# Optimization experiments

Measured on AMD Instinct MI355X. Metric: run time of the kernel, lower is better.

Reference implementation:

```python
import jax, jax.numpy as jnp
import numpy as np
import math

N, C_IN, H, W = 8, 256, 64, 64
C_ATT, C_OUT = 128, 256
BN_EPS = 1e-5


def conv_bn_relu(x, w, gamma, beta, mean, var):
    # 1x1 conv (no bias) + BatchNorm (eval mode) + ReLU
    y = jnp.einsum('oc,nchw->nohw', w, x)
    inv = gamma / jnp.sqrt(var + BN_EPS)
    y = y * inv[None, :, None, None] + (beta - mean * inv)[None, :, None, None]
    return jax.nn.relu(y)


def setup_inputs() -> dict:
    key = jax.random.key(0)
    ks = jax.random.split(key, 12)
    x = jax.random.normal(ks[0], (N, C_IN, H, W), dtype=jnp.float32)
    mask = jnp.ones((N, 1, H, W), dtype=jnp.float32)
    reduc_w = jax.random.normal(ks[1], (C_OUT, C_IN), dtype=jnp.float32) * (1.0 / math.sqrt(C_IN))
    reduc_gamma = jnp.ones((C_OUT,), dtype=jnp.float32)
    reduc_beta = jnp.zeros((C_OUT,), dtype=jnp.float32)
    reduc_mean = jax.random.normal(ks[2], (C_OUT,), dtype=jnp.float32) * 0.1
    reduc_var = jax.random.uniform(ks[3], (C_OUT,), dtype=jnp.float32) + 0.5
    att_w = jax.random.normal(ks[4], (C_ATT, C_IN), dtype=jnp.float32) * (1.0 / math.sqrt(C_IN))
    att_gamma = jnp.ones((C_ATT,), dtype=jnp.float32)
    att_beta = jnp.zeros((C_ATT,), dtype=jnp.float32)
    att_mean = jax.random.normal(ks[5], (C_ATT,), dtype=jnp.float32) * 0.1
    att_var = jax.random.uniform(ks[6], (C_ATT,), dtype=jnp.float32) + 0.5
    return {
        'x': x, 'mask': mask,
        'reduc_w': reduc_w, 'reduc_gamma': reduc_gamma, 'reduc_beta': reduc_beta,
        'reduc_mean': reduc_mean, 'reduc_var': reduc_var,
        'att_w': att_w, 'att_gamma': att_gamma, 'att_beta': att_beta,
        'att_mean': att_mean, 'att_var': att_var,
    }


def reference(x, mask, reduc_w, reduc_gamma, reduc_beta, reduc_mean, reduc_var,
              att_w, att_gamma, att_beta, att_mean, att_var):
    n, _, h, w = x.shape
    x_feat = conv_bn_relu(x, reduc_w, reduc_gamma, reduc_beta, reduc_mean, reduc_var)   # [n,C_OUT,h,w]
    x_atten = conv_bn_relu(x, att_w, att_gamma, att_beta, att_mean, att_var)            # [n,C_ATT,h,w]
    c = x_atten.shape[1]
    q = x_atten.reshape(n, c, h * w)                                                    # [n,c,HW]
    # energy[n,i,j] = sum_c q[n,c,i]*q[n,c,j] / (1e-8 + sqrt(c))
    energy = jnp.einsum('nci,ncj->nij', q, q) / (1e-8 + math.sqrt(c))
    energy = energy + (mask.reshape(n, 1, h * w) - 1.0) * 1e8
    weight = jax.nn.softmax(energy, axis=2)                                             # [n,HW,HW]
    feat = x_feat.reshape(n, x_feat.shape[1], h * w)                                    # [n,C_OUT,HW]
    out = jnp.einsum('nij,ncj->nci', weight, feat)                                      # [n,C_OUT,HW]
    out = out.reshape(n, feat.shape[1], h, w)
    out = out * mask
    return out
```

## Files before the change

### kernel.cpp

```cpp
#include <hip/hip_runtime.h>
#include <cstdint>
#include <cstddef>

#define NB 8
#define CIN 256
#define HWX 4096
#define CF 256
#define CA 128
#define CT 384

typedef __attribute__((ext_vector_type(8))) _Float16 half8;
typedef __attribute__((ext_vector_type(8))) short short8;
typedef __attribute__((ext_vector_type(4))) float f32x4;
typedef __attribute__((ext_vector_type(4))) unsigned int u32x4;

#define OFF_W    0
#define OFF_BIAS (CT*CIN*4)
#define OFF_FEAT (OFF_BIAS + 2048)
#define OFF_Q    (OFF_FEAT + NB*CF*HWX*2)
#define OFF_NORM (OFF_Q + NB*HWX*CA*2)
#define OFF_G    (OFF_NORM + NB*HWX*4)

__device__ inline unsigned short f16_bits(float f) {
  _Float16 h = (_Float16)f;
  return __builtin_bit_cast(unsigned short, h);
}
__device__ inline half8 ld_half8(const unsigned short* p) {
  short8 r = *(const short8*)p;
  return __builtin_bit_cast(half8, r);
}

__device__ inline void g2l16(const void* g, void* l) {
  __builtin_amdgcn_global_load_lds(
      (const __attribute__((address_space(1))) unsigned int*)g,
      (__attribute__((address_space(3))) unsigned int*)l, 16, 0, 0);
}

__global__ __launch_bounds__(256) void fold_bn_k(
    const float* __restrict__ rw, const float* __restrict__ rg,
    const float* __restrict__ rb, const float* __restrict__ rm, const float* __restrict__ rv,
    const float* __restrict__ aw, const float* __restrict__ ag,
    const float* __restrict__ ab2, const float* __restrict__ am, const float* __restrict__ av,
    float* __restrict__ wf, float* __restrict__ bias, unsigned* __restrict__ Gmax) {
  int o = blockIdx.x, k = threadIdx.x;
  if (o == 0 && k < NB) Gmax[k] = 0u;
  const float* wsrc; float g, b, m, v;
  if (o < CF) { wsrc = rw + (size_t)o*CIN; g = rg[o]; b = rb[o]; m = rm[o]; v = rv[o]; }
  else { int oa = o - CF; wsrc = aw + (size_t)oa*CIN; g = ag[oa]; b = ab2[oa]; m = am[oa]; v = av[oa]; }
  float inv = g / sqrtf(v + 1e-5f);
  wf[(size_t)o*CIN + k] = wsrc[k] * inv;
  if (k == 0) bias[o] = b - m*inv;
}

__global__ __launch_bounds__(256) void conv_k(
    const float* __restrict__ x, const float* __restrict__ wf,
    const float* __restrict__ bias, unsigned short* __restrict__ feat,
    unsigned short* __restrict__ q, float* __restrict__ normq,
    unsigned* __restrict__ Gmax) {
  __shared__ float w_s[16][132];
  __shared__ float x_s[16][132];
  __shared__ float normS[128];
  int b = blockIdx.x;
  int n = b / 96, rem = b % 96;
  int ot = rem / 32, pt = rem % 32;
  int oc0 = ot*128, p0 = pt*128;
  int t = threadIdx.x, ty = t >> 4, tx = t & 15;
  const float* xn = x + (size_t)n*CIN*HWX;
  float acc[8][8];
  #pragma unroll
  for (int i=0;i<8;i++)
    #pragma unroll
    for (int j=0;j<8;j++) acc[i][j]=0.f;

  for (int k0=0; k0<CIN; k0+=16) {
    __syncthreads();
    #pragma unroll
    for (int pass=0; pass<2; pass++) {
      int idx = pass*256+t, oc = idx>>2, kq = idx&3;
      f32x4 wv = *(const f32x4*)(wf + (size_t)(oc0+oc)*CIN + k0 + kq*4);
      w_s[kq*4+0][oc]=wv.x; w_s[kq*4+1][oc]=wv.y; w_s[kq*4+2][oc]=wv.z; w_s[kq*4+3][oc]=wv.w;
    }
    #pragma unroll
    for (int pass=0; pass<2; pass++) {
      int idx = pass*256+t, row = idx>>5, cc = idx&31;
      f32x4 xv = *(const f32x4*)(xn + (size_t)(k0+row)*HWX + p0 + cc*4);
      *(f32x4*)&x_s[row][cc*4] = xv;
    }
    __syncthreads();
    #pragma unroll
    for (int kk=0; kk<16; kk++) {
      float a[8], bb[8];
      *(f32x4*)&a[0]  = *(const f32x4*)&w_s[kk][ty*8];
      *(f32x4*)&a[4]  = *(const f32x4*)&w_s[kk][ty*8+4];
      *(f32x4*)&bb[0] = *(const f32x4*)&x_s[kk][tx*8];
      *(f32x4*)&bb[4] = *(const f32x4*)&x_s[kk][tx*8+4];
      #pragma unroll
      for (int i=0;i<8;i++)
        #pragma unroll
        for (int j=0;j<8;j++) acc[i][j] = fmaf(a[i], bb[j], acc[i][j]);
    }
  }

  int posb = p0 + tx*8;
  float bs[8];
  #pragma unroll
  for (int i=0;i<8;i++) bs[i] = bias[oc0 + ty*8 + i];

  if (oc0 < CF) {
    #pragma unroll
    for (int i=0;i<8;i++) {
      int oc = oc0 + ty*8 + i;
      alignas(16) unsigned short u[8];
      #pragma unroll
      for (int j=0;j<8;j++) {
        float vv = fmaxf(acc[i][j] + bs[i], 0.f);
        u[j] = f16_bits(vv);
      }
      *(u32x4*)(feat + (size_t)n*CF*HWX + (size_t)oc*HWX + posb) = *(const u32x4*)u;
    }
  } else {
    __syncthreads();
    if (t < 128) normS[t] = 0.f;
    __syncthreads();
    int cb = oc0 - CF + ty*8;
    float ns[8];
    #pragma unroll
    for (int j=0;j<8;j++) {
      alignas(16) unsigned short uh[8];
      float s2 = 0.f;
      #pragma unroll
      for (int i=0;i<8;i++) {
        float vv = fmaxf(acc[i][j] + bs[i], 0.f);
        uh[i] = f16_bits(vv);
        s2 += vv*vv;
      }
      ns[j] = s2;
      *(u32x4*)(q + ((size_t)n*HWX + posb + j)*CA + cb) = *(const u32x4*)uh;
    }
    #pragma unroll
    for (int j=0;j<8;j++) atomicAdd(&normS[tx*8+j], ns[j]);
    __syncthreads();
    if (t < 128) {
      float nv = sqrtf(normS[t]);
      normq[(size_t)n*HWX + p0 + t] = nv;
      atomicMax(Gmax + n, __float_as_uint(nv));
    }
  }
}

__global__ __launch_bounds__(256, 3) void flash_k(
    const unsigned short* __restrict__ q, const unsigned short* __restrict__ feat,
    const float* __restrict__ mask, const float* __restrict__ normq,
    const unsigned* __restrict__ Gmax, float* __restrict__ out) {
  __shared__ alignas(16) unsigned short sQ[64*128];
  __shared__ alignas(16) unsigned short sP[64][72];
  __shared__ float sM[64];
  int b = blockIdx.x;
  int n = b & 7, it = b >> 3;
  int i0 = it * 64;
  int t = threadIdx.x;
  int w = t >> 6, lane = t & 63, quad = lane >> 4, col = lane & 15;
  const unsigned short* q_n = q + (size_t)n*HWX*CA;
  const unsigned short* f_n = feat + (size_t)n*CF*HWX;
  const float* m_n = mask + (size_t)n*HWX;
  const int rloc = t >> 4, oct16 = t & 15;
  const float inv_s = 1.0f/(1e-8f + sqrtf(128.0f));

  auto stage_Q = [&](int j0) {
    #pragma unroll
    for (int c=0;c<4;c++) {
      int row = c*16 + rloc;
      int og = oct16 ^ (row & 15);
      g2l16(q_n + (size_t)(j0+row)*CA + og*8, &sQ[(size_t)row*128 + oct16*8]);
    }
    if (t < 16) g2l16(m_n + j0 + t*4, &sM[t*4]);
  };

  half8 ah[4];
  {
    int arow = i0 + w*16 + col;
    #pragma unroll
    for (int ks=0; ks<4; ks++)
      ah[ks] = ld_half8(q_n + (size_t)arow*CA + ks*32 + quad*8);
  }
  float Gn = __uint_as_float(Gmax[n]);
  float cvals[4];
  #pragma unroll
  for (int r=0;r<4;r++)
    cvals[r] = normq[(size_t)n*HWX + i0 + w*16 + quad*4 + r] * Gn * inv_s - 5.0f;

  f32x4 fzero = {0.f,0.f,0.f,0.f};
  f32x4 o[4][4];
  #pragma unroll
  for (int ig=0;ig<4;ig++)
    #pragma unroll
    for (int ct=0;ct<4;ct++) o[ig][ct] = fzero;
  float lrun[4] = {0.f,0.f,0.f,0.f};

  stage_Q(0);
  for (int ji = 0; ji < 64; ji++) {
    int j0 = ji*64;
    __syncthreads();

    f32x4 s[4];
    #pragma unroll
    for (int jt=0;jt<4;jt++) s[jt] = fzero;
    #pragma unroll
    for (int jt=0;jt<4;jt++) {
      int row = jt*16 + col;
      #pragma unroll
      for (int ks=0; ks<4; ks++) {
        int slot = (ks*4 + quad) ^ (row & 15);
        half8 bq = ld_half8(&sQ[row*128 + slot*8]);
        s[jt] = __builtin_amdgcn_mfma_f32_16x16x32_f16(ah[ks], bq, s[jt], 0, 0, 0);
      }
    }

    #pragma unroll
    for (int jt=0;jt<4;jt++) {
      float mj = (sM[jt*16+col] - 1.f) * 1e8f;
      #pragma unroll
      for (int r=0;r<4;r++) {
        float p = __expf(s[jt][r]*inv_s + mj - cvals[r]);
        lrun[r] += p;
        sP[w*16 + quad*4 + r][jt*16 + col] = f16_bits(p);
      }
    }

    __syncthreads();
    if (ji + 1 < 64) stage_Q(j0+64);

    #pragma unroll
    for (int ks2=0; ks2<2; ks2++) {
      half8 aP[4];
      #pragma unroll
      for (int ig=0;ig<4;ig++)
        aP[ig] = ld_half8(&sP[ig*16 + col][ks2*32 + quad*8]);
      half8 bF[4];
      #pragma unroll
      for (int ct=0;ct<4;ct++) {
        int c = w*64 + ct*16 + col;
        bF[ct] = ld_half8(f_n + (size_t)c*HWX + j0 + ks2*32 + quad*8);
      }
      #pragma unroll
      for (int ct=0;ct<4;ct++)
        #pragma unroll
        for (int ig=0;ig<4;ig++)
          o[ig][ct] = __builtin_amdgcn_mfma_f32_16x16x32_f16(aP[ig], bF[ct], o[ig][ct], 0, 0, 0);
    }
  }

  #pragma unroll
  for (int r=0;r<4;r++) {
    float ss = lrun[r];
    ss += __shfl_xor(ss, 1, 64);
    ss += __shfl_xor(ss, 2, 64);
    ss += __shfl_xor(ss, 4, 64);
    ss += __shfl_xor(ss, 8, 64);
    lrun[r] = ss;
  }
  __syncthreads();
  #pragma unroll
  for (int r=0;r<4;r++)
    if (col == 0) sM[w*16 + quad*4 + r] = lrun[r];
  __syncthreads();
  #pragma unroll
  for (int ig=0;ig<4;ig++) {
    f32x4 lv = *(const f32x4*)&sM[ig*16 + quad*4];
    f32x4 mv = *(const f32x4*)(m_n + i0 + ig*16 + quad*4);
    f32x4 minv;
    #pragma unroll
    for (int r=0;r<4;r++) minv[r] = mv[r] / lv[r];
    #pragma unroll
    for (int ct=0;ct<4;ct++) {
      int c = w*64 + ct*16 + col;
      f32x4 v;
      #pragma unroll
      for (int r=0;r<4;r++) v[r] = o[ig][ct][r] * minv[r];
      *(f32x4*)(out + ((size_t)n*CF + c)*HWX + i0 + ig*16 + quad*4) = v;
    }
  }
}

extern "C" void kernel_launch(void* const* d_in, const int* in_sizes, int n_in,
                              void* d_out, int out_size, void* d_ws, size_t ws_size,
                              hipStream_t stream) {
  const float* x    = (const float*)d_in[0];
  const float* mask = (const float*)d_in[1];
  const float* rw   = (const float*)d_in[2];
  const float* rg   = (const float*)d_in[3];
  const float* rb   = (const float*)d_in[4];
  const float* rm   = (const float*)d_in[5];
  const float* rv   = (const float*)d_in[6];
  const float* aw   = (const float*)d_in[7];
  const float* ag   = (const float*)d_in[8];
  const float* ab   = (const float*)d_in[9];
  const float* am   = (const float*)d_in[10];
  const float* av   = (const float*)d_in[11];
  float* out = (float*)d_out;
  char* ws = (char*)d_ws;
  float* wf   = (float*)(ws + OFF_W);
  float* bias = (float*)(ws + OFF_BIAS);
  unsigned short* feat = (unsigned short*)(ws + OFF_FEAT);
  unsigned short* q    = (unsigned short*)(ws + OFF_Q);
  float* normq = (float*)(ws + OFF_NORM);
  unsigned* Gmax = (unsigned*)(ws + OFF_G);

  hipLaunchKernelGGL(fold_bn_k, dim3(CT), dim3(CIN), 0, stream,
                     rw, rg, rb, rm, rv, aw, ag, ab, am, av, wf, bias, Gmax);
  hipLaunchKernelGGL(conv_k, dim3(768), dim3(256), 0, stream,
                     x, wf, bias, feat, q, normq, Gmax);
  hipLaunchKernelGGL(flash_k, dim3(512), dim3(256), 0, stream,
                     q, feat, mask, normq, Gmax, out);
}
```

Before: 339.1 us.

## Move 1x1 conv to fp16 MFMA and split flash work across 8 waves

The conv kernel now uses fp16 MFMA on x and weights staged in LDS, with BN folded into fp16 weights. Each block computes all 384 output channels for 64 pixels, and writes feat and q through LDS for coalesced stores. The q norm is now a shuffle reduction. The flash kernel moves to 512 threads, so each wave holds half the score columns and 32 output channels, and feature loads are hoisted ahead of the score MFMAs. fp16 inputs to the conv reduce accuracy, and the larger flash block may cut occupancy.

New measurement: 295.2 us. 1.15x faster.

```diff
diff --git a/kernel.cpp b/kernel.cpp
--- a/kernel.cpp
+++ b/kernel.cpp
@@ -14,9 +14,9 @@
 typedef __attribute__((ext_vector_type(4))) float f32x4;
 typedef __attribute__((ext_vector_type(4))) unsigned int u32x4;
 
-#define OFF_W    0
-#define OFF_BIAS (CT*CIN*4)
-#define OFF_FEAT (OFF_BIAS + 2048)
+#define OFF_WH   0
+#define OFF_BIAS (CT*CIN*2)
+#define OFF_FEAT (OFF_BIAS + CT*4)
 #define OFF_Q    (OFF_FEAT + NB*CF*HWX*2)
 #define OFF_NORM (OFF_Q + NB*HWX*CA*2)
 #define OFF_G    (OFF_NORM + NB*HWX*4)
@@ -41,135 +41,143 @@
     const float* __restrict__ rb, const float* __restrict__ rm, const float* __restrict__ rv,
     const float* __restrict__ aw, const float* __restrict__ ag,
     const float* __restrict__ ab2, const float* __restrict__ am, const float* __restrict__ av,
-    float* __restrict__ wf, float* __restrict__ bias, unsigned* __restrict__ Gmax) {
+    unsigned short* __restrict__ wh, float* __restrict__ bias, unsigned* __restrict__ Gmax) {
   int o = blockIdx.x, k = threadIdx.x;
   if (o == 0 && k < NB) Gmax[k] = 0u;
   const float* wsrc; float g, b, m, v;
   if (o < CF) { wsrc = rw + (size_t)o*CIN; g = rg[o]; b = rb[o]; m = rm[o]; v = rv[o]; }
   else { int oa = o - CF; wsrc = aw + (size_t)oa*CIN; g = ag[oa]; b = ab2[oa]; m = am[oa]; v = av[oa]; }
   float inv = g / sqrtf(v + 1e-5f);
-  wf[(size_t)o*CIN + k] = wsrc[k] * inv;
+  wh[(size_t)o*CIN + k] = f16_bits(wsrc[k] * inv);
   if (k == 0) bias[o] = b - m*inv;
 }
 
-__global__ __launch_bounds__(256) void conv_k(
-    const float* __restrict__ x, const float* __restrict__ wf,
+__global__ __launch_bounds__(256, 2) void conv_k(
+    const float* __restrict__ x, const unsigned short* __restrict__ wh,
     const float* __restrict__ bias, unsigned short* __restrict__ feat,
     unsigned short* __restrict__ q, float* __restrict__ normq,
     unsigned* __restrict__ Gmax) {
-  __shared__ float w_s[16][132];
-  __shared__ float x_s[16][132];
-  __shared__ float normS[128];
+  __shared__ unsigned short sBuf[18432];
+  __shared__ unsigned short sQr[64*136];
   int b = blockIdx.x;
-  int n = b / 96, rem = b % 96;
-  int ot = rem / 32, pt = rem % 32;
-  int oc0 = ot*128, p0 = pt*128;
-  int t = threadIdx.x, ty = t >> 4, tx = t & 15;
+  int n = b & 7, pt0 = b >> 3;
+  int p0 = pt0 * 64;
+  int t = threadIdx.x;
+  int w = t >> 6, lane = t & 63, quad = lane >> 4, col = lane & 15;
   const float* xn = x + (size_t)n*CIN*HWX;
-  float acc[8][8];
-  #pragma unroll
-  for (int i=0;i<8;i++)
-    #pragma unroll
-    for (int j=0;j<8;j++) acc[i][j]=0.f;
-
-  for (int k0=0; k0<CIN; k0+=16) {
-    __syncthreads();
-    #pragma unroll
-    for (int pass=0; pass<2; pass++) {
-      int idx = pass*256+t, oc = idx>>2, kq = idx&3;
-      f32x4 wv = *(const f32x4*)(wf + (size_t)(oc0+oc)*CIN + k0 + kq*4);
-      w_s[kq*4+0][oc]=wv.x; w_s[kq*4+1][oc]=wv.y; w_s[kq*4+2][oc]=wv.z; w_s[kq*4+3][oc]=wv.w;
-    }
-    #pragma unroll
-    for (int pass=0; pass<2; pass++) {
-      int idx = pass*256+t, row = idx>>5, cc = idx&31;
-      f32x4 xv = *(const f32x4*)(xn + (size_t)(k0+row)*HWX + p0 + cc*4);
-      *(f32x4*)&x_s[row][cc*4] = xv;
-    }
-    __syncthreads();
-    #pragma unroll
-    for (int kk=0; kk<16; kk++) {
-      float a[8], bb[8];
-      *(f32x4*)&a[0]  = *(const f32x4*)&w_s[kk][ty*8];
-      *(f32x4*)&a[4]  = *(const f32x4*)&w_s[kk][ty*8+4];
-      *(f32x4*)&bb[0] = *(const f32x4*)&x_s[kk][tx*8];
-      *(f32x4*)&bb[4] = *(const f32x4*)&x_s[kk][tx*8+4];
-      #pragma unroll
-      for (int i=0;i<8;i++)
-        #pragma unroll
-        for (int j=0;j<8;j++) acc[i][j] = fmaf(a[i], bb[j], acc[i][j]);
-    }
-  }
-
-  int posb = p0 + tx*8;
-  float bs[8];
-  #pragma unroll
-  for (int i=0;i<8;i++) bs[i] = bias[oc0 + ty*8 + i];
-
-  if (oc0 < CF) {
-    #pragma unroll
-    for (int i=0;i<8;i++) {
-      int oc = oc0 + ty*8 + i;
-      alignas(16) unsigned short u[8];
-      #pragma unroll
-      for (int j=0;j<8;j++) {
-        float vv = fmaxf(acc[i][j] + bs[i], 0.f);
-        u[j] = f16_bits(vv);
+
+  #pragma unroll
+  for (int pass=0; pass<8; pass++) {
+    int idx = pass*256 + t;
+    int kp = idx >> 4, pq = idx & 15;
+    f32x4 a = *(const f32x4*)(xn + (size_t)(2*kp)*HWX + p0 + pq*4);
+    f32x4 c = *(const f32x4*)(xn + (size_t)(2*kp+1)*HWX + p0 + pq*4);
+    #pragma unroll
+    for (int j=0;j<4;j++) {
+      int pos = pq*4 + j;
+      unsigned dd = (unsigned)f16_bits(a[j]) | ((unsigned)f16_bits(c[j]) << 16);
+      *(unsigned*)&sBuf[pos*264 + kp*2] = dd;
+    }
+  }
+  __syncthreads();
+
+  f32x4 fzero = {0.f,0.f,0.f,0.f};
+  f32x4 acc[4][6];
+  #pragma unroll
+  for (int pt=0;pt<4;pt++)
+    #pragma unroll
+    for (int ot=0;ot<6;ot++) acc[pt][ot] = fzero;
+
+  #pragma unroll
+  for (int ks=0; ks<8; ks++) {
+    half8 B6[6];
+    #pragma unroll
+    for (int ot=0;ot<6;ot++)
+      B6[ot] = ld_half8(wh + (size_t)(w*96 + ot*16 + col)*CIN + ks*32 + quad*8);
+    half8 A4[4];
+    #pragma unroll
+    for (int pt=0;pt<4;pt++)
+      A4[pt] = ld_half8(&sBuf[(pt*16+col)*264 + ks*32 + quad*8]);
+    #pragma unroll
+    for (int pt=0;pt<4;pt++)
+      #pragma unroll
+      for (int ot=0;ot<6;ot++)
+        acc[pt][ot] = __builtin_amdgcn_mfma_f32_16x16x32_f16(A4[pt], B6[ot], acc[pt][ot], 0, 0, 0);
+  }
+  __syncthreads();
+
+  float bv[6];
+  #pragma unroll
+  for (int ot=0;ot<6;ot++) bv[ot] = bias[w*96 + ot*16 + col];
+  #pragma unroll
+  for (int pt=0;pt<4;pt++)
+    #pragma unroll
+    for (int ot=0;ot<6;ot++) {
+      int oc = w*96 + ot*16 + col;
+      #pragma unroll
+      for (int r=0;r<4;r++) {
+        float v = fmaxf(acc[pt][ot][r] + bv[ot], 0.f);
+        int pos = pt*16 + quad*4 + r;
+        if (oc < CF) sBuf[oc*72 + pos] = f16_bits(v);
+        else         sQr[pos*136 + (oc - CF)] = f16_bits(v);
       }
-      *(u32x4*)(feat + (size_t)n*CF*HWX + (size_t)oc*HWX + posb) = *(const u32x4*)u;
-    }
-  } else {
-    __syncthreads();
-    if (t < 128) normS[t] = 0.f;
-    __syncthreads();
-    int cb = oc0 - CF + ty*8;
-    float ns[8];
-    #pragma unroll
-    for (int j=0;j<8;j++) {
-      alignas(16) unsigned short uh[8];
-      float s2 = 0.f;
-      #pragma unroll
-      for (int i=0;i<8;i++) {
-        float vv = fmaxf(acc[i][j] + bs[i], 0.f);
-        uh[i] = f16_bits(vv);
-        s2 += vv*vv;
-      }
-      ns[j] = s2;
-      *(u32x4*)(q + ((size_t)n*HWX + posb + j)*CA + cb) = *(const u32x4*)uh;
-    }
-    #pragma unroll
-    for (int j=0;j<8;j++) atomicAdd(&normS[tx*8+j], ns[j]);
-    __syncthreads();
-    if (t < 128) {
-      float nv = sqrtf(normS[t]);
-      normq[(size_t)n*HWX + p0 + t] = nv;
+    }
+  __syncthreads();
+
+  {
+    const unsigned short* src = &sBuf[t*72];
+    unsigned short* dst = feat + (size_t)n*CF*HWX + (size_t)t*HWX + p0;
+    #pragma unroll
+    for (int s=0;s<8;s++)
+      *(u32x4*)(dst + s*8) = *(const u32x4*)(src + s*8);
+  }
+  {
+    int pos = t >> 2, seg = t & 3;
+    const unsigned short* src = &sQr[pos*136 + seg*32];
+    unsigned short* dst = q + ((size_t)n*HWX + p0 + pos)*CA + seg*32;
+    float s2 = 0.f;
+    #pragma unroll
+    for (int u=0;u<4;u++) {
+      short8 v = *(const short8*)(src + u*8);
+      *(short8*)(dst + u*8) = v;
+      half8 h = __builtin_bit_cast(half8, v);
+      #pragma unroll
+      for (int e=0;e<8;e++) { float fe = (float)h[e]; s2 += fe*fe; }
+    }
+    s2 += __shfl_xor(s2, 1, 64);
+    s2 += __shfl_xor(s2, 2, 64);
+    if (seg == 0) {
+      float nv = sqrtf(s2);
+      normq[(size_t)n*HWX + p0 + pos] = nv;
       atomicMax(Gmax + n, __float_as_uint(nv));
     }
   }
 }
 
-__global__ __launch_bounds__(256, 3) void flash_k(
+__global__ __launch_bounds__(512, 4) void flash_k(
     const unsigned short* __restrict__ q, const unsigned short* __restrict__ feat,
     const float* __restrict__ mask, const float* __restrict__ normq,
     const unsigned* __restrict__ Gmax, float* __restrict__ out) {
   __shared__ alignas(16) unsigned short sQ[64*128];
   __shared__ alignas(16) unsigned short sP[64][72];
   __shared__ float sM[64];
+  __shared__ float sL[2][64];
   int b = blockIdx.x;
   int n = b & 7, it = b >> 3;
   int i0 = it * 64;
   int t = threadIdx.x;
   int w = t >> 6, lane = t & 63, quad = lane >> 4, col = lane & 15;
+  int wq = w & 3, wh = w >> 2;
   const unsigned short* q_n = q + (size_t)n*HWX*CA;
   const unsigned short* f_n = feat + (size_t)n*CF*HWX;
   const float* m_n = mask + (size_t)n*HWX;
-  const int rloc = t >> 4, oct16 = t & 15;
+  const int rloc = (t >> 4) & 31, oct16 = t & 15;
   const float inv_s = 1.0f/(1e-8f + sqrtf(128.0f));
 
   auto stage_Q = [&](int j0) {
     #pragma unroll
-    for (int c=0;c<4;c++) {
-      int row = c*16 + rloc;
+    for (int c=0;c<2;c++) {
+      int row = c*32 + rloc;
       int og = oct16 ^ (row & 15);
       g2l16(q_n + (size_t)(j0+row)*CA + og*8, &sQ[(size_t)row*128 + oct16*8]);
     }
@@ -178,7 +186,7 @@
 
   half8 ah[4];
   {
-    int arow = i0 + w*16 + col;
+    int arow = i0 + wq*16 + col;
     #pragma unroll
     for (int ks=0; ks<4; ks++)
       ah[ks] = ld_half8(q_n + (size_t)arow*CA + ks*32 + quad*8);
@@ -187,14 +195,12 @@
   float cvals[4];
   #pragma unroll
   for (int r=0;r<4;r++)
-    cvals[r] = normq[(size_t)n*HWX + i0 + w*16 + quad*4 + r] * Gn * inv_s - 5.0f;
+    cvals[r] = normq[(size_t)n*HWX + i0 + wq*16 + quad*4 + r] * Gn * inv_s - 5.0f;
 
   f32x4 fzero = {0.f,0.f,0.f,0.f};
-  f32x4 o[4][4];
-  #pragma unroll
-  for (int ig=0;ig<4;ig++)
-    #pragma unroll
-    for (int ct=0;ct<4;ct++) o[ig][ct] = fzero;
+  f32x4 o[4][2];
+  #pragma unroll
+  for (int ig=0;ig<4;ig++) { o[ig][0] = fzero; o[ig][1] = fzero; }
   float lrun[4] = {0.f,0.f,0.f,0.f};
 
   stage_Q(0);
@@ -202,28 +208,36 @@
     int j0 = ji*64;
     __syncthreads();
 
-    f32x4 s[4];
-    #pragma unroll
-    for (int jt=0;jt<4;jt++) s[jt] = fzero;
-    #pragma unroll
-    for (int jt=0;jt<4;jt++) {
-      int row = jt*16 + col;
+    half8 bF[2][2];
+    #pragma unroll
+    for (int ks2=0;ks2<2;ks2++)
+      #pragma unroll
+      for (int ct=0;ct<2;ct++) {
+        int c = w*32 + ct*16 + col;
+        bF[ks2][ct] = ld_half8(f_n + (size_t)c*HWX + j0 + ks2*32 + quad*8);
+      }
+
+    f32x4 s[2];
+    s[0] = fzero; s[1] = fzero;
+    #pragma unroll
+    for (int jt=0;jt<2;jt++) {
+      int rowj = wh*32 + jt*16 + col;
       #pragma unroll
       for (int ks=0; ks<4; ks++) {
-        int slot = (ks*4 + quad) ^ (row & 15);
-        half8 bq = ld_half8(&sQ[row*128 + slot*8]);
+        int slot = (ks*4 + quad) ^ (rowj & 15);
+        half8 bq = ld_half8(&sQ[rowj*128 + slot*8]);
         s[jt] = __builtin_amdgcn_mfma_f32_16x16x32_f16(ah[ks], bq, s[jt], 0, 0, 0);
       }
     }
 
     #pragma unroll
-    for (int jt=0;jt<4;jt++) {
-      float mj = (sM[jt*16+col] - 1.f) * 1e8f;
+    for (int jt=0;jt<2;jt++) {
+      float mj = (sM[wh*32 + jt*16 + col] - 1.f) * 1e8f;
       #pragma unroll
       for (int r=0;r<4;r++) {
         float p = __expf(s[jt][r]*inv_s + mj - cvals[r]);
         lrun[r] += p;
-        sP[w*16 + quad*4 + r][jt*16 + col] = f16_bits(p);
+        sP[wq*16 + quad*4 + r][wh*32 + jt*16 + col] = f16_bits(p);
       }
     }
 
@@ -236,17 +250,11 @@
       #pragma unroll
       for (int ig=0;ig<4;ig++)
         aP[ig] = ld_half8(&sP[ig*16 + col][ks2*32 + quad*8]);
-      half8 bF[4];
-      #pragma unroll
-      for (int ct=0;ct<4;ct++) {
-        int c = w*64 + ct*16 + col;
-        bF[ct] = ld_half8(f_n + (size_t)c*HWX + j0 + ks2*32 + quad*8);
-      }
-      #pragma unroll
-      for (int ct=0;ct<4;ct++)
+      #pragma unroll
+      for (int ct=0;ct<2;ct++)
         #pragma unroll
         for (int ig=0;ig<4;ig++)
-          o[ig][ct] = __builtin_amdgcn_mfma_f32_16x16x32_f16(aP[ig], bF[ct], o[ig][ct], 0, 0, 0);
+          o[ig][ct] = __builtin_amdgcn_mfma_f32_16x16x32_f16(aP[ig], bF[ks2][ct], o[ig][ct], 0, 0, 0);
     }
   }
 
@@ -259,25 +267,26 @@
     ss += __shfl_xor(ss, 8, 64);
     lrun[r] = ss;
   }
+  #pragma unroll
+  for (int r=0;r<4;r++)
+    if (col == 0) sL[wh][wq*16 + quad*4 + r] = lrun[r];
   __syncthreads();
   #pragma unroll
-  for (int r=0;r<4;r++)
-    if (col == 0) sM[w*16 + quad*4 + r] = lrun[r];
-  __syncthreads();
-  #pragma unroll
   for (int ig=0;ig<4;ig++) {
-    f32x4 lv = *(const f32x4*)&sM[ig*16 + quad*4];
-    f32x4 mv = *(const f32x4*)(m_n + i0 + ig*16 + quad*4);
+    int base = ig*16 + quad*4;
+    f32x4 l0 = *(const f32x4*)&sL[0][base];
+    f32x4 l1 = *(const f32x4*)&sL[1][base];
+    f32x4 mv = *(const f32x4*)(m_n + i0 + base);
     f32x4 minv;
     #pragma unroll
-    for (int r=0;r<4;r++) minv[r] = mv[r] / lv[r];
-    #pragma unroll
-    for (int ct=0;ct<4;ct++) {
-      int c = w*64 + ct*16 + col;
+    for (int r=0;r<4;r++) minv[r] = mv[r] / (l0[r] + l1[r]);
+    #pragma unroll
+    for (int ct=0;ct<2;ct++) {
+      int c = w*32 + ct*16 + col;
       f32x4 v;
       #pragma unroll
       for (int r=0;r<4;r++) v[r] = o[ig][ct][r] * minv[r];
-      *(f32x4*)(out + ((size_t)n*CF + c)*HWX + i0 + ig*16 + quad*4) = v;
+      *(f32x4*)(out + ((size_t)n*CF + c)*HWX + i0 + base) = v;
     }
   }
 }
@@ -299,7 +308,7 @@
   const float* av   = (const float*)d_in[11];
   float* out = (float*)d_out;
   char* ws = (char*)d_ws;
-  float* wf   = (float*)(ws + OFF_W);
+  unsigned short* wh = (unsigned short*)(ws + OFF_WH);
   float* bias = (float*)(ws + OFF_BIAS);
   unsigned short* feat = (unsigned short*)(ws + OFF_FEAT);
   unsigned short* q    = (unsigned short*)(ws + OFF_Q);
@@ -307,9 +316,9 @@
   unsigned* Gmax = (unsigned*)(ws + OFF_G);
 
   hipLaunchKernelGGL(fold_bn_k, dim3(CT), dim3(CIN), 0, stream,
-                     rw, rg, rb, rm, rv, aw, ag, ab, am, av, wf, bias, Gmax);
-  hipLaunchKernelGGL(conv_k, dim3(768), dim3(256), 0, stream,
-                     x, wf, bias, feat, q, normq, Gmax);
-  hipLaunchKernelGGL(flash_k, dim3(512), dim3(256), 0, stream,
+                     rw, rg, rb, rm, rv, aw, ag, ab, am, av, wh, bias, Gmax);
+  hipLaunchKernelGGL(conv_k, dim3(512), dim3(256), 0, stream,
+                     x, wh, bias, feat, q, normq, Gmax);
+  hipLaunchKernelGGL(flash_k, dim3(512), dim3(512), 0, stream,
                      q, feat, mask, normq, Gmax, out);
 }
```
